# Kernel tuning notes

Hardware: AMD Instinct MI355X
Metric: run time of the kernel (lower is better)

## Reference

```python
import jax, jax.numpy as jnp
import numpy as np

N_NODES = 100000
N_EDGES = 625000
EMB_DIM = 128
ALPHA = 0.8  # alpha in original; effective scale is alpha/2 = 0.4


def setup_inputs() -> dict:
    key = jax.random.key(0)
    k1, k2, k3, k4, k5 = jax.random.split(key, 5)
    x = jax.random.normal(k1, (N_NODES, EMB_DIM), dtype=jnp.float32)
    e = jax.random.normal(k2, (N_NODES, EMB_DIM), dtype=jnp.float32)
    hg_vals = jax.random.uniform(k3, (N_EDGES,), dtype=jnp.float32)
    hg_rows = jax.random.randint(k4, (N_EDGES,), 0, N_NODES, dtype=jnp.int32)
    hg_cols = jax.random.randint(k5, (N_EDGES,), 0, N_NODES, dtype=jnp.int32)
    t = jnp.zeros((), dtype=jnp.float32)
    return {"t": t, "x": x, "e": e, "hg_vals": hg_vals,
            "hg_rows": hg_rows, "hg_cols": hg_cols}


def reference(t, x, e, hg_vals, hg_rows, hg_cols):
    # f = spmm((alpha/2) * HG, x) - x + e, with alpha = 0.8 (constant per entry)
    n = x.shape[0]
    scale = ALPHA / 2.0
    # gather source node features per nonzero, scale by edge value
    msgs = (scale * hg_vals)[:, None] * x[hg_cols]          # [nnz, d]
    prop = jax.ops.segment_sum(msgs, hg_rows, num_segments=n)  # [N, d]
    return prop - x + e
```

## Files before the change

### kernel.cpp

```cpp
#include <hip/hip_runtime.h>
#include <hip/hip_fp16.h>


#define EMB_DIM 128
#define Q_SLOTS 32
#define CAP 32
#define OVF_MAX 4096

struct __align__(8) half4_t { __half2 a, b; };

__global__ void prep_kernel(const int* __restrict__ rows,
                            const int* __restrict__ cols,
                            const float* __restrict__ vals,
                            int* __restrict__ counts,
                            int2* __restrict__ slots,
                            int* __restrict__ ovf_cursor,
                            int4* __restrict__ ovf,
                            int n_edges,
                            const float4* __restrict__ x4,
                            half4_t* __restrict__ xh4,
                            int n_x4) {
    int i = blockIdx.x * blockDim.x + threadIdx.x;
    if (i < n_x4) {
        float4 f = x4[i];
        half4_t h;
        h.a = __floats2half2_rn(f.x, f.y);
        h.b = __floats2half2_rn(f.z, f.w);
        xh4[i] = h;
    }
    if (i < n_edges) {
        int r = rows[i];
        int2 p;
        p.x = cols[i];
        p.y = __float_as_int(0.4f * vals[i]);
        int pos = atomicAdd(&counts[r], 1);
        if (pos < CAP) {
            slots[(size_t)r * CAP + pos] = p;
        } else {
            int o = atomicAdd(ovf_cursor, 1);
            if (o < OVF_MAX) ovf[o] = make_int4(r, p.x, p.y, 0);
        }
    }
}

__global__ void gather_fp16_kernel(const half4_t* __restrict__ xh4,
                                   const float4* __restrict__ e4,
                                   const int* __restrict__ counts,
                                   const int2* __restrict__ slots,
                                   float4* __restrict__ out4, int n_nodes) {
    int tid = blockIdx.x * blockDim.x + threadIdx.x;
    int row = tid >> 5;
    int q   = tid & 31;
    if (row >= n_nodes) return;

    int n = counts[row];
    n = (n < CAP) ? n : CAP;
    const int2* b = slots + (size_t)row * CAP;

    int2 myp = make_int2(0, 0);
    if (q < n) myp = b[q];

    float4 acc = make_float4(0.f, 0.f, 0.f, 0.f);
    int nm1 = n - 1;

    for (int base = 0; base < n; base += 8) {
        int   col[8];
        float v[8];
#pragma unroll
        for (int k = 0; k < 8; ++k) {
            int j  = base + k;
            int jc = (j < n) ? j : nm1;
            col[k] = __shfl(myp.x, jc, 32);
            int vi = __shfl(myp.y, jc, 32);
            v[k]   = (j < n) ? __int_as_float(vi) : 0.f;
        }
        half4_t hv[8];
#pragma unroll
        for (int k = 0; k < 8; ++k) {
            hv[k] = xh4[col[k] * Q_SLOTS + q];
        }
#pragma unroll
        for (int k = 0; k < 8; ++k) {
            float2 f0 = __half22float2(hv[k].a);
            float2 f1 = __half22float2(hv[k].b);
            acc.x = fmaf(v[k], f0.x, acc.x);
            acc.y = fmaf(v[k], f0.y, acc.y);
            acc.z = fmaf(v[k], f1.x, acc.z);
            acc.w = fmaf(v[k], f1.y, acc.w);
        }
    }

    int idx = row * Q_SLOTS + q;
    half4_t hx = xh4[idx];
    float2 x0 = __half22float2(hx.a);
    float2 x1 = __half22float2(hx.b);
    float4 er = e4[idx];
    out4[idx] = make_float4(acc.x + er.x - x0.x,
                            acc.y + er.y - x0.y,
                            acc.z + er.z - x1.x,
                            acc.w + er.w - x1.y);
}

__global__ void gather_f32_kernel(const float4* __restrict__ x4,
                                  const float4* __restrict__ e4,
                                  const int* __restrict__ counts,
                                  const int2* __restrict__ slots,
                                  float4* __restrict__ out4, int n_nodes) {
    int tid = blockIdx.x * blockDim.x + threadIdx.x;
    int row = tid >> 5;
    int q   = tid & 31;
    if (row >= n_nodes) return;

    int n = counts[row];
    n = (n < CAP) ? n : CAP;
    const int2* b = slots + (size_t)row * CAP;

    int2 myp = make_int2(0, 0);
    if (q < n) myp = b[q];

    float4 acc = make_float4(0.f, 0.f, 0.f, 0.f);
    int nm1 = n - 1;

    for (int base = 0; base < n; base += 8) {
        int   col[8];
        float v[8];
#pragma unroll
        for (int k = 0; k < 8; ++k) {
            int j  = base + k;
            int jc = (j < n) ? j : nm1;
            col[k] = __shfl(myp.x, jc, 32);
            int vi = __shfl(myp.y, jc, 32);
            v[k]   = (j < n) ? __int_as_float(vi) : 0.f;
        }
        float4 xv[8];
#pragma unroll
        for (int k = 0; k < 8; ++k) {
            xv[k] = x4[col[k] * Q_SLOTS + q];
        }
#pragma unroll
        for (int k = 0; k < 8; ++k) {
            acc.x = fmaf(v[k], xv[k].x, acc.x);
            acc.y = fmaf(v[k], xv[k].y, acc.y);
            acc.z = fmaf(v[k], xv[k].z, acc.z);
            acc.w = fmaf(v[k], xv[k].w, acc.w);
        }
    }

    int idx = row * Q_SLOTS + q;
    float4 xr = x4[idx];
    float4 er = e4[idx];
    out4[idx] = make_float4(acc.x + er.x - xr.x,
                            acc.y + er.y - xr.y,
                            acc.z + er.z - xr.z,
                            acc.w + er.w - xr.w);
}

__global__ void ovf_fix_kernel(const int* __restrict__ ovf_cursor,
                               const int4* __restrict__ ovf,
                               const float* __restrict__ x,
                               float* __restrict__ out) {
    int tid = blockIdx.x * blockDim.x + threadIdx.x;
    int k = tid >> 5;
    int q = tid & 31;
    int cnt = *ovf_cursor;
    cnt = (cnt < OVF_MAX) ? cnt : OVF_MAX;
    if (k >= cnt) return;
    int4 en = ovf[k];
    float v = __int_as_float(en.z);
    float4 m = ((const float4*)(x + (size_t)en.y * EMB_DIM))[q];
    float* o = out + (size_t)en.x * EMB_DIM + q * 4;
    atomicAdd(o + 0, v * m.x);
    atomicAdd(o + 1, v * m.y);
    atomicAdd(o + 2, v * m.z);
    atomicAdd(o + 3, v * m.w);
}

__global__ void build_chain_kernel(const int* __restrict__ rows,
                                   const int* __restrict__ cols,
                                   const float* __restrict__ vals,
                                   int* __restrict__ head,
                                   int4* __restrict__ nodes, int n_edges) {
    int i = blockIdx.x * blockDim.x + threadIdx.x;
    if (i >= n_edges) return;
    int r = rows[i];
    int prev = atomicExch(&head[r], i);
    nodes[i] = make_int4(cols[i], __float_as_int(0.4f * vals[i]), prev, 0);
}
__global__ void gather_chain_kernel(const float2* __restrict__ x2,
                                    const float2* __restrict__ e2,
                                    const int* __restrict__ head,
                                    const int4* __restrict__ nodes,
                                    float2* __restrict__ out2, int n_nodes) {
    int tid = blockIdx.x * blockDim.x + threadIdx.x;
    int row = tid >> 6, q = tid & 63;
    if (row >= n_nodes) return;
    float2 acc = make_float2(0.f, 0.f);
    int j = head[row];
    if (j >= 0) {
        int4 nd = nodes[j];
        for (;;) {
            int4 nd2;
            bool more = (nd.z >= 0);
            if (more) nd2 = nodes[nd.z];
            float v = __int_as_float(nd.y);
            float2 xv = x2[nd.x * 64 + q];
            acc.x = fmaf(v, xv.x, acc.x);
            acc.y = fmaf(v, xv.y, acc.y);
            if (!more) break;
            nd = nd2;
        }
    }
    int idx = row * 64 + q;
    float2 xr = x2[idx], er = e2[idx];
    out2[idx] = make_float2(acc.x + er.x - xr.x, acc.y + er.y - xr.y);
}

extern "C" void kernel_launch(void* const* d_in, const int* in_sizes, int n_in,
                              void* d_out, int out_size, void* d_ws, size_t ws_size,
                              hipStream_t stream) {
    const float* x    = (const float*)d_in[1];
    const float* e    = (const float*)d_in[2];
    const float* vals = (const float*)d_in[3];
    const int*   rows = (const int*)d_in[4];
    const int*   cols = (const int*)d_in[5];
    float* out = (float*)d_out;

    const int n_edges = in_sizes[3];
    const int n_nodes = in_sizes[1] / EMB_DIM;
    const int n_x4    = n_nodes * Q_SLOTS;

    size_t need_a = (size_t)OVF_MAX * sizeof(int4) +
                    (size_t)n_x4 * sizeof(half4_t) +
                    (size_t)n_nodes * CAP * sizeof(int2) +
                    (size_t)(n_nodes + 1) * sizeof(int);
    size_t need_b = (size_t)OVF_MAX * sizeof(int4) +
                    (size_t)n_nodes * CAP * sizeof(int2) +
                    (size_t)(n_nodes + 1) * sizeof(int);

    if (ws_size >= need_a) {
        int4*    ovf        = (int4*)d_ws;
        half4_t* xh4        = (half4_t*)(ovf + OVF_MAX);
        int2*    slots      = (int2*)(xh4 + (size_t)n_x4);
        int*     counts     = (int*)(slots + (size_t)n_nodes * CAP);
        int*     ovf_cursor = counts + n_nodes;

        hipMemsetAsync(counts, 0, (size_t)(n_nodes + 1) * sizeof(int), stream);

        int pt = (n_x4 > n_edges) ? n_x4 : n_edges;
        int pb = (pt + 255) / 256;
        prep_kernel<<<pb, 256, 0, stream>>>(rows, cols, vals, counts, slots,
                                            ovf_cursor, ovf, n_edges,
                                            (const float4*)x, xh4, n_x4);

        long long gt = (long long)n_nodes * 32;
        int gb = (int)((gt + 255) / 256);
        gather_fp16_kernel<<<gb, 256, 0, stream>>>(xh4, (const float4*)e,
                                                   counts, slots,
                                                   (float4*)out, n_nodes);

        int ob = (OVF_MAX * 32 + 255) / 256;
        ovf_fix_kernel<<<ob, 256, 0, stream>>>(ovf_cursor, ovf, x, out);
    } else if (ws_size >= need_b) {
        int4* ovf        = (int4*)d_ws;
        int2* slots      = (int2*)(ovf + OVF_MAX);
        int*  counts     = (int*)(slots + (size_t)n_nodes * CAP);
        int*  ovf_cursor = counts + n_nodes;

        hipMemsetAsync(counts, 0, (size_t)(n_nodes + 1) * sizeof(int), stream);

        int eb = (n_edges + 255) / 256;
        prep_kernel<<<eb, 256, 0, stream>>>(rows, cols, vals, counts, slots,
                                            ovf_cursor, ovf, n_edges,
                                            (const float4*)x, (half4_t*)0, 0);

        long long gt = (long long)n_nodes * 32;
        int gb = (int)((gt + 255) / 256);
        gather_f32_kernel<<<gb, 256, 0, stream>>>((const float4*)x,
                                                  (const float4*)e,
                                                  counts, slots,
                                                  (float4*)out, n_nodes);

        int ob = (OVF_MAX * 32 + 255) / 256;
        ovf_fix_kernel<<<ob, 256, 0, stream>>>(ovf_cursor, ovf, x, out);
    } else {
        int4* nodes = (int4*)d_ws;
        int*  head  = (int*)(nodes + n_edges);
        hipMemsetAsync(head, 0xFF, (size_t)n_nodes * sizeof(int), stream);
        int eb = (n_edges + 255) / 256;
        build_chain_kernel<<<eb, 256, 0, stream>>>(rows, cols, vals, head,
                                                   nodes, n_edges);
        long long gt = (long long)n_nodes * 64;
        int gb = (int)((gt + 255) / 256);
        gather_chain_kernel<<<gb, 256, 0, stream>>>((const float2*)x,
                                                    (const float2*)e,
                                                    head, nodes,
                                                    (float2*)out, n_nodes);
    }
}
```

Before: 213.2 us.

## Fold overflow handling into gather kernel, halve slot cap, use nontemporal memory ops

The separate overflow fix kernel with float atomics is removed. Rows whose degree exceeds the bucket capacity now scan the overflow list inside the gather kernel. The per-row slot capacity drops from 32 to 16, which shrinks the slot buffer and its traffic, and the overflow list grows to 8192 entries. Streaming loads and stores of edges, e and out use nontemporal builtins. The risk is that high-degree rows serially scan the whole overflow list, which causes wave divergence, and the list may now overflow its cap at average degree 6.25.

```diff
diff --git a/kernel.cpp b/kernel.cpp
--- a/kernel.cpp
+++ b/kernel.cpp
@@ -4,10 +4,11 @@
 
 #define EMB_DIM 128
 #define Q_SLOTS 32
-#define CAP 32
-#define OVF_MAX 4096
+#define CAP 16
+#define OVF_MAX 8192
 
 struct __align__(8) half4_t { __half2 a, b; };
+typedef float f32x4 __attribute__((ext_vector_type(4)));
 
 __global__ void prep_kernel(const int* __restrict__ rows,
                             const int* __restrict__ cols,
@@ -17,22 +18,24 @@
                             int* __restrict__ ovf_cursor,
                             int4* __restrict__ ovf,
                             int n_edges,
-                            const float4* __restrict__ x4,
+                            const f32x4* __restrict__ x4,
                             half4_t* __restrict__ xh4,
                             int n_x4) {
     int i = blockIdx.x * blockDim.x + threadIdx.x;
     if (i < n_x4) {
-        float4 f = x4[i];
+        f32x4 f = __builtin_nontemporal_load(x4 + i);
         half4_t h;
         h.a = __floats2half2_rn(f.x, f.y);
         h.b = __floats2half2_rn(f.z, f.w);
         xh4[i] = h;
     }
     if (i < n_edges) {
-        int r = rows[i];
+        int   r  = __builtin_nontemporal_load(rows + i);
+        int   c  = __builtin_nontemporal_load(cols + i);
+        float vv = __builtin_nontemporal_load(vals + i);
         int2 p;
-        p.x = cols[i];
-        p.y = __float_as_int(0.4f * vals[i]);
+        p.x = c;
+        p.y = __float_as_int(0.4f * vv);
         int pos = atomicAdd(&counts[r], 1);
         if (pos < CAP) {
             slots[(size_t)r * CAP + pos] = p;
@@ -44,21 +47,25 @@
 }
 
 __global__ void gather_fp16_kernel(const half4_t* __restrict__ xh4,
-                                   const float4* __restrict__ e4,
+                                   const f32x4* __restrict__ e4,
                                    const int* __restrict__ counts,
                                    const int2* __restrict__ slots,
-                                   float4* __restrict__ out4, int n_nodes) {
+                                   const int* __restrict__ ovf_cursor,
+                                   const int4* __restrict__ ovf,
+                                   f32x4* __restrict__ out4, int n_nodes) {
     int tid = blockIdx.x * blockDim.x + threadIdx.x;
     int row = tid >> 5;
     int q   = tid & 31;
     if (row >= n_nodes) return;
 
-    int n = counts[row];
-    n = (n < CAP) ? n : CAP;
-    const int2* b = slots + (size_t)row * CAP;
-
-    int2 myp = make_int2(0, 0);
-    if (q < n) myp = b[q];
+    int cfull = counts[row];
+    int n = (cfull < CAP) ? cfull : CAP;
+    const long long* b = (const long long*)(slots + (size_t)row * CAP);
+
+    long long pp = 0;
+    if (q < n) pp = __builtin_nontemporal_load(b + q);
+    int myc = (int)(pp & 0xffffffffLL);
+    int myv = (int)(pp >> 32);
 
     float4 acc = make_float4(0.f, 0.f, 0.f, 0.f);
     int nm1 = n - 1;
@@ -70,8 +77,8 @@
         for (int k = 0; k < 8; ++k) {
             int j  = base + k;
             int jc = (j < n) ? j : nm1;
-            col[k] = __shfl(myp.x, jc, 32);
-            int vi = __shfl(myp.y, jc, 32);
+            col[k] = __shfl(myc, jc, 32);
+            int vi = __shfl(myv, jc, 32);
             v[k]   = (j < n) ? __int_as_float(vi) : 0.f;
         }
         half4_t hv[8];
@@ -90,33 +97,57 @@
         }
     }
 
+    if (cfull > CAP) {
+        int cnt = *ovf_cursor;
+        cnt = (cnt < OVF_MAX) ? cnt : OVF_MAX;
+        for (int k = 0; k < cnt; ++k) {
+            int4 en = ovf[k];
+            if (en.x == row) {
+                float vv = __int_as_float(en.z);
+                half4_t hv = xh4[en.y * Q_SLOTS + q];
+                float2 f0 = __half22float2(hv.a);
+                float2 f1 = __half22float2(hv.b);
+                acc.x = fmaf(vv, f0.x, acc.x);
+                acc.y = fmaf(vv, f0.y, acc.y);
+                acc.z = fmaf(vv, f1.x, acc.z);
+                acc.w = fmaf(vv, f1.y, acc.w);
+            }
+        }
+    }
+
     int idx = row * Q_SLOTS + q;
     half4_t hx = xh4[idx];
     float2 x0 = __half22float2(hx.a);
     float2 x1 = __half22float2(hx.b);
-    float4 er = e4[idx];
-    out4[idx] = make_float4(acc.x + er.x - x0.x,
-                            acc.y + er.y - x0.y,
-                            acc.z + er.z - x1.x,
-                            acc.w + er.w - x1.y);
-}
-
-__global__ void gather_f32_kernel(const float4* __restrict__ x4,
-                                  const float4* __restrict__ e4,
+    f32x4 er = __builtin_nontemporal_load(e4 + idx);
+    f32x4 o;
+    o.x = acc.x + er.x - x0.x;
+    o.y = acc.y + er.y - x0.y;
+    o.z = acc.z + er.z - x1.x;
+    o.w = acc.w + er.w - x1.y;
+    __builtin_nontemporal_store(o, out4 + idx);
+}
+
+__global__ void gather_f32_kernel(const f32x4* __restrict__ x4,
+                                  const f32x4* __restrict__ e4,
                                   const int* __restrict__ counts,
                                   const int2* __restrict__ slots,
-                                  float4* __restrict__ out4, int n_nodes) {
+                                  const int* __restrict__ ovf_cursor,
+                                  const int4* __restrict__ ovf,
+                                  f32x4* __restrict__ out4, int n_nodes) {
     int tid = blockIdx.x * blockDim.x + threadIdx.x;
     int row = tid >> 5;
     int q   = tid & 31;
     if (row >= n_nodes) return;
 
-    int n = counts[row];
-    n = (n < CAP) ? n : CAP;
-    const int2* b = slots + (size_t)row * CAP;
-
-    int2 myp = make_int2(0, 0);
-    if (q < n) myp = b[q];
+    int cfull = counts[row];
+    int n = (cfull < CAP) ? cfull : CAP;
+    const long long* b = (const long long*)(slots + (size_t)row * CAP);
+
+    long long pp = 0;
+    if (q < n) pp = __builtin_nontemporal_load(b + q);
+    int myc = (int)(pp & 0xffffffffLL);
+    int myv = (int)(pp >> 32);
 
     float4 acc = make_float4(0.f, 0.f, 0.f, 0.f);
     int nm1 = n - 1;
@@ -128,11 +159,11 @@
         for (int k = 0; k < 8; ++k) {
             int j  = base + k;
             int jc = (j < n) ? j : nm1;
-            col[k] = __shfl(myp.x, jc, 32);
-            int vi = __shfl(myp.y, jc, 32);
+            col[k] = __shfl(myc, jc, 32);
+            int vi = __shfl(myv, jc, 32);
             v[k]   = (j < n) ? __int_as_float(vi) : 0.f;
         }
-        float4 xv[8];
+        f32x4 xv[8];
 #pragma unroll
         for (int k = 0; k < 8; ++k) {
             xv[k] = x4[col[k] * Q_SLOTS + q];
@@ -146,33 +177,31 @@
         }
     }
 
+    if (cfull > CAP) {
+        int cnt = *ovf_cursor;
+        cnt = (cnt < OVF_MAX) ? cnt : OVF_MAX;
+        for (int k = 0; k < cnt; ++k) {
+            int4 en = ovf[k];
+            if (en.x == row) {
+                float vv = __int_as_float(en.z);
+                f32x4 m = x4[en.y * Q_SLOTS + q];
+                acc.x = fmaf(vv, m.x, acc.x);
+                acc.y = fmaf(vv, m.y, acc.y);
+                acc.z = fmaf(vv, m.z, acc.z);
+                acc.w = fmaf(vv, m.w, acc.w);
+            }
+        }
+    }
+
     int idx = row * Q_SLOTS + q;
-    float4 xr = x4[idx];
-    float4 er = e4[idx];
-    out4[idx] = make_float4(acc.x + er.x - xr.x,
-                            acc.y + er.y - xr.y,
-                            acc.z + er.z - xr.z,
-                            acc.w + er.w - xr.w);
-}
-
-__global__ void ovf_fix_kernel(const int* __restrict__ ovf_cursor,
-                               const int4* __restrict__ ovf,
-                               const float* __restrict__ x,
-                               float* __restrict__ out) {
-    int tid = blockIdx.x * blockDim.x + threadIdx.x;
-    int k = tid >> 5;
-    int q = tid & 31;
-    int cnt = *ovf_cursor;
-    cnt = (cnt < OVF_MAX) ? cnt : OVF_MAX;
-    if (k >= cnt) return;
-    int4 en = ovf[k];
-    float v = __int_as_float(en.z);
-    float4 m = ((const float4*)(x + (size_t)en.y * EMB_DIM))[q];
-    float* o = out + (size_t)en.x * EMB_DIM + q * 4;
-    atomicAdd(o + 0, v * m.x);
-    atomicAdd(o + 1, v * m.y);
-    atomicAdd(o + 2, v * m.z);
-    atomicAdd(o + 3, v * m.w);
+    f32x4 xr = x4[idx];
+    f32x4 er = __builtin_nontemporal_load(e4 + idx);
+    f32x4 o;
+    o.x = acc.x + er.x - xr.x;
+    o.y = acc.y + er.y - xr.y;
+    o.z = acc.z + er.z - xr.z;
+    o.w = acc.w + er.w - xr.w;
+    __builtin_nontemporal_store(o, out4 + idx);
 }
 
 __global__ void build_chain_kernel(const int* __restrict__ rows,
@@ -250,16 +279,14 @@
         int pb = (pt + 255) / 256;
         prep_kernel<<<pb, 256, 0, stream>>>(rows, cols, vals, counts, slots,
                                             ovf_cursor, ovf, n_edges,
-                                            (const float4*)x, xh4, n_x4);
+                                            (const f32x4*)x, xh4, n_x4);
 
         long long gt = (long long)n_nodes * 32;
         int gb = (int)((gt + 255) / 256);
-        gather_fp16_kernel<<<gb, 256, 0, stream>>>(xh4, (const float4*)e,
+        gather_fp16_kernel<<<gb, 256, 0, stream>>>(xh4, (const f32x4*)e,
                                                    counts, slots,
-                                                   (float4*)out, n_nodes);
-
-        int ob = (OVF_MAX * 32 + 255) / 256;
-        ovf_fix_kernel<<<ob, 256, 0, stream>>>(ovf_cursor, ovf, x, out);
+                                                   ovf_cursor, ovf,
+                                                   (f32x4*)out, n_nodes);
     } else if (ws_size >= need_b) {
         int4* ovf        = (int4*)d_ws;
         int2* slots      = (int2*)(ovf + OVF_MAX);
@@ -271,17 +298,15 @@
         int eb = (n_edges + 255) / 256;
         prep_kernel<<<eb, 256, 0, stream>>>(rows, cols, vals, counts, slots,
                                             ovf_cursor, ovf, n_edges,
-                                            (const float4*)x, (half4_t*)0, 0);
+                                            (const f32x4*)x, (half4_t*)0, 0);
 
         long long gt = (long long)n_nodes * 32;
         int gb = (int)((gt + 255) / 256);
-        gather_f32_kernel<<<gb, 256, 0, stream>>>((const float4*)x,
-                                                  (const float4*)e,
+        gather_f32_kernel<<<gb, 256, 0, stream>>>((const f32x4*)x,
+                                                  (const f32x4*)e,
                                                   counts, slots,
-                                                  (float4*)out, n_nodes);
-
-        int ob = (OVF_MAX * 32 + 255) / 256;
-        ovf_fix_kernel<<<ob, 256, 0, stream>>>(ovf_cursor, ovf, x, out);
+                                                  ovf_cursor, ovf,
+                                                  (f32x4*)out, n_nodes);
     } else {
         int4* nodes = (int4*)d_ws;
         int*  head  = (int*)(nodes + n_edges);
```

After: 209.1 us. Within noise of the previous version (-1.9%).
